# Optimization experiments

Hardware: AMD Instinct MI355X
Metric: run time of the kernel (lower is better)

## Reference

```python
import jax, jax.numpy as jnp
import numpy as np

B, N, F_IN, F_OUT, H = 8, 1024, 128, 64, 4
EPS = 1e-7
NEG_SLOPE = 0.2


def setup_inputs() -> dict:
    key = jax.random.key(0)
    k_a, k_x, k_w, k_aw, k_ab = jax.random.split(key, 5)
    A = jax.random.randint(k_a, (B, N, N), 0, 2).astype(jnp.float32)
    x = jax.random.normal(k_x, (B, N, F_IN), dtype=jnp.float32)
    # per-head params (stacked over head axis): GAT.W (xavier-normal-ish), attention Linear(2F->1)
    W = jax.random.normal(k_w, (H, F_IN, F_OUT), dtype=jnp.float32) * np.sqrt(2.0 / (F_IN + F_OUT))
    lim = 1.0 / np.sqrt(2 * F_OUT)
    a_w = jax.random.uniform(k_aw, (H, 2 * F_OUT), minval=-lim, maxval=lim, dtype=jnp.float32)
    a_b = jax.random.uniform(k_ab, (H,), minval=-lim, maxval=lim, dtype=jnp.float32)
    return {"A": A, "x": x, "W": W, "a_w": a_w, "a_b": a_b}


def reference(A, x, W, a_w, a_b):
    # Wh: (B, H, N, F_OUT)
    Wh = jnp.einsum('bnf,hfo->bhno', x, W)
    # attention linear on concat([Wh_i, Wh_j]) is separable: a1.Wh_i + a2.Wh_j + b
    a1, a2 = a_w[:, :F_OUT], a_w[:, F_OUT:]
    s_i = jnp.einsum('bhno,ho->bhn', Wh, a1)   # depends on row index i (dim 1 of (B,N,N))
    s_j = jnp.einsum('bhno,ho->bhn', Wh, a2)   # depends on col index j (dim 2)
    e = s_i[:, :, :, None] + s_j[:, :, None, :] + a_b[None, :, None, None]  # (B,H,Ni,Nj)
    e = jnp.where(e >= 0, e, NEG_SLOPE * e)  # LeakyReLU(0.2)
    # masked softmax as in source: exp, mask by A, normalize over dim=1 of (B,N,N) -> axis 2 here
    exps = jnp.exp(e) * A[:, None, :, :]
    attn = exps / (jnp.sum(exps, axis=2, keepdims=True) + EPS)
    out = jnp.einsum('bhij,bhjo->bhio', attn, Wh)  # matmul over j
    # concat heads on feature dim: (B, N, H*F_OUT)
    return out.transpose(0, 2, 1, 3).reshape(B, N, H * F_OUT)
```

## Files before the change

kernel.cpp:

```cpp
#include <hip/hip_runtime.h>
#include <hip/hip_bf16.h>
#include <hip/hip_fp16.h>

#define BB 8
#define NN 1024
#define FIN 128
#define FOUT 64
#define HH 4
#define EPSV 1e-7f
#define SLOPE 0.2f
#define LOG2E 1.44269504088896340736f

typedef _Float16 v8h __attribute__((ext_vector_type(8)));
typedef _Float16 v4h __attribute__((ext_vector_type(4)));
typedef _Float16 v2h __attribute__((ext_vector_type(2)));
typedef __fp16 v2hf __attribute__((ext_vector_type(2)));
typedef float v4f __attribute__((ext_vector_type(4)));

union U8 { v2h p[4]; v8h v; };
union U2 { v2hf hf; v2h h; };

__device__ __forceinline__ v2h clamp01(v2h x) {
  v2h zero = {(_Float16)0.0f, (_Float16)0.0f};
  v2h one = {(_Float16)1.0f, (_Float16)1.0f};
  return __builtin_elementwise_min(__builtin_elementwise_max(x, zero), one);
}

__device__ __forceinline__ v2h cvt2(float a, float b) {
  U2 u;
  u.hf = __builtin_amdgcn_cvt_pkrtz(a, b);
  return u.h;
}

__device__ __forceinline__ float dot2(v2h a, v2h b, float c) {
  U2 ua, ub;
  ua.h = a;
  ub.h = b;
  return __builtin_amdgcn_fdot2(ua.hf, ub.hf, c, false);
}

__global__ __launch_bounds__(256) void k0_wt(const float* __restrict__ W,
                                             _Float16* __restrict__ Wtt) {
  for (int it = 0; it < 16; ++it) {
    int idx = blockIdx.x * 4096 + it * 256 + threadIdx.x;
    int e = idx & 7, ln = (idx >> 3) & 15, kgg = (idx >> 7) & 15,
        ct = idx >> 11;
    int c = ct * 16 + ln, k = kgg * 8 + e;
    Wtt[idx] = (_Float16)W[(size_t)(c >> 6) * 8192 + k * 64 + (c & 63)];
  }
}

__global__ __launch_bounds__(256) void k1_whm(
    const float* __restrict__ x, const _Float16* __restrict__ Wtt,
    const float* __restrict__ aw, const float* __restrict__ ab,
    _Float16* __restrict__ WhH, float* __restrict__ si2,
    _Float16* __restrict__ tjh, _Float16* __restrict__ djh,
    _Float16* __restrict__ e2jh, float* __restrict__ e2i_t,
    float* __restrict__ di_t) {
  __shared__ _Float16 xs[16][136];
  int tid = threadIdx.x;
#pragma unroll
  for (int t2 = 0; t2 < 2; ++t2) {
    int idx = t2 * 256 + tid;
    int row = idx >> 5, c4 = (idx & 31) * 4;
    float4 v = *(const float4*)(x + ((size_t)blockIdx.x * 16 + row) * FIN + c4);
    v4h hv;
    hv[0] = (_Float16)v.x; hv[1] = (_Float16)v.y;
    hv[2] = (_Float16)v.z; hv[3] = (_Float16)v.w;
    *(v4h*)(&xs[row][c4]) = hv;
  }
  __syncthreads();
  int w = tid >> 6, l = tid & 63;
  int kg = l >> 4, ln = l & 15;
  v4f acc[4] = {{}, {}, {}, {}};
#pragma unroll
  for (int ks = 0; ks < 4; ++ks) {
    v8h af = *(const v8h*)(&xs[ln][ks * 32 + kg * 8]);
    int kgg = ks * 4 + kg;
#pragma unroll
    for (int t = 0; t < 4; ++t) {
      int ct = w * 4 + t;
      v8h bf = *(const v8h*)(Wtt + (((size_t)ct * 16 + kgg) * 16 + ln) * 8);
      acc[t] = __builtin_amdgcn_mfma_f32_16x16x32_f16(af, bf, acc[t], 0, 0, 0);
    }
  }
  float a1v[4], a2v[4];
#pragma unroll
  for (int t = 0; t < 4; ++t) {
    a1v[t] = aw[w * 128 + t * 16 + ln];
    a2v[t] = aw[w * 128 + 64 + t * 16 + ln];
  }
  float abv = ab[w];
#pragma unroll
  for (int r = 0; r < 4; ++r) {
    float v1 = acc[0][r] * a1v[0] + acc[1][r] * a1v[1] +
               acc[2][r] * a1v[2] + acc[3][r] * a1v[3];
    float v2 = acc[0][r] * a2v[0] + acc[1][r] * a2v[1] +
               acc[2][r] * a2v[2] + acc[3][r] * a2v[3];
#pragma unroll
    for (int off = 1; off < 16; off <<= 1) {
      v1 += __shfl_xor(v1, off);
      v2 += __shfl_xor(v2, off);
    }
    if (ln == 0) {
      int gr = blockIdx.x * 16 + kg * 4 + r;
      int b_ = gr >> 10, n_ = gr & 1023;
      size_t row = ((size_t)b_ * HH + w) * NN + n_;
      float v1L = v1 * LOG2E;
      float tjL = (v2 + abv) * LOG2E;
      si2[row] = v1L;
      float e1i = __builtin_amdgcn_exp2f(v1L);
      float e2i = __builtin_amdgcn_exp2f(0.2f * v1L);
      e2i_t[row] = e2i;
      di_t[row] = e1i - e2i;
      float e1j = __builtin_amdgcn_exp2f(tjL);
      float e2j = __builtin_amdgcn_exp2f(0.2f * tjL);
      tjh[row] = (_Float16)tjL;
      e2jh[row] = (_Float16)e2j;
      djh[row] = (_Float16)(e1j - e2j);
    }
  }
#pragma unroll
  for (int t = 0; t < 4; ++t) {
#pragma unroll
    for (int r = 0; r < 4; ++r) {
      int gr = blockIdx.x * 16 + kg * 4 + r;
      int b_ = gr >> 10, n_ = gr & 1023;
      WhH[(((size_t)b_ * HH + w) * NN + n_) * 64 + (t * 16 + ln)] =
          (_Float16)acc[t][r];
    }
  }
}

__global__ __launch_bounds__(256) void kb_colsum_bits(
    const float* __restrict__ A, const float* __restrict__ si2,
    const float* __restrict__ e2i_t, const float* __restrict__ di_t,
    const _Float16* __restrict__ tjh, const _Float16* __restrict__ djh,
    const _Float16* __restrict__ e2jh, float* __restrict__ part,
    unsigned long long* __restrict__ Abits) {
  __shared__ v2h si_p[4][16], di_p[4][16], e2i_p[4][16];
  int b = blockIdx.z, is = blockIdx.y, jt = blockIdx.x;
  int tid = threadIdx.x;
  int w = tid >> 6, lane = tid & 63;
  int j = jt * 256 + tid;
  int i0 = is * 32;
  if (tid < 64) {
    int h = tid >> 4, pp = tid & 15;
    size_t row = ((size_t)(b * HH + h)) * NN + i0 + 2 * pp;
    si_p[h][pp] = cvt2(si2[row], si2[row + 1]);
    di_p[h][pp] = cvt2(di_t[row], di_t[row + 1]);
    e2i_p[h][pp] = cvt2(e2i_t[row], e2i_t[row + 1]);
  }
  __syncthreads();
  v2h tjb[4], djb[4], ejb[4];
#pragma unroll
  for (int h = 0; h < 4; ++h) {
    size_t jr = ((size_t)(b * HH + h)) * NN + j;
    _Float16 t = tjh[jr], d = djh[jr], e = e2jh[jr];
    tjb[h][0] = t; tjb[h][1] = t;
    djb[h][0] = d; djb[h][1] = d;
    ejb[h][0] = e; ejb[h][1] = e;
  }
  v2h big = {(_Float16)4096.0f, (_Float16)4096.0f};
  float acc[4] = {0.f, 0.f, 0.f, 0.f};
  const float* Ap = A + ((size_t)b * NN + i0) * NN + j;
  unsigned long long myword = 0ull;
#pragma unroll
  for (int c = 0; c < 4; ++c) {
    float av[8];
#pragma unroll
    for (int q = 0; q < 8; ++q) av[q] = Ap[(size_t)(c * 8 + q) * NN];
    v2h apk[4];
#pragma unroll
    for (int q = 0; q < 4; ++q) apk[q] = cvt2(av[2 * q], av[2 * q + 1]);
#pragma unroll
    for (int q = 0; q < 8; ++q) {
      unsigned long long m = __ballot(av[q] != 0.0f);
      if (lane == c * 8 + q) myword = m;
    }
#pragma unroll
    for (int h = 0; h < 4; ++h) {
      U8 si4, di4, ei4;
      si4.v = *(const v8h*)&si_p[h][c * 4];
      di4.v = *(const v8h*)&di_p[h][c * 4];
      ei4.v = *(const v8h*)&e2i_p[h][c * 4];
#pragma unroll
      for (int pp = 0; pp < 4; ++pp) {
        v2h f = si4.p[pp] + tjb[h];
        v2h s = clamp01(f * big);
        v2h ei = s * di4.p[pp] + ei4.p[pp];
        v2h ej = s * djb[h] + ejb[h];
        v2h p = ei * ej;
        acc[h] = dot2(p, apk[pp], acc[h]);
      }
    }
  }
  if (lane < 32)
    Abits[((size_t)b * NN + i0 + lane) * 16 + jt * 4 + w] = myword;
#pragma unroll
  for (int h = 0; h < 4; ++h)
    part[((size_t)(is * 32) + b * HH + h) * NN + j] = acc[h];
}

__global__ __launch_bounds__(256) void k3_scale_tr(
    const _Float16* __restrict__ WhH, const float* __restrict__ part,
    _Float16* __restrict__ VTt) {
  __shared__ float rbuf[64];
  __shared__ _Float16 tile[64 * 66];
  int bid = blockIdx.x;
  int b = bid & 7, rest = bid >> 3;
  int h = rest & 3, jt = rest >> 2;
  int bh = b * HH + h, j0 = jt * 64;
  int tid = threadIdx.x;
  if (tid < 64) {
    float s = 0.f;
#pragma unroll
    for (int is = 0; is < 32; ++is)
      s += part[((size_t)(is * 32) + bh) * NN + j0 + tid];
    rbuf[tid] = 1.0f / (s + EPSV);
  }
  __syncthreads();
#pragma unroll
  for (int it = 0; it < 16; ++it) {
    int lin = it * 256 + tid;
    int jj = lin >> 6, o = lin & 63;
    float v = (float)WhH[((size_t)bh * NN + j0 + jj) * 64 + o] * rbuf[jj];
    tile[o * 66 + jj] = (_Float16)v;
  }
  __syncthreads();
#pragma unroll
  for (int it = 0; it < 16; ++it) {
    int lin = it * 256 + tid;
    int o = lin >> 6, jj64 = lin & 63;
    int j = j0 + jj64;
    int jb = j >> 5, jj = j & 31;
    VTt[(((size_t)bh * 32 + jb) * 64 + o) * 32 + jj] = tile[o * 66 + jj64];
  }
}

__global__ __launch_bounds__(512, 4) void k4_pv(
    const unsigned long long* __restrict__ Abits,
    const float* __restrict__ si2, const _Float16* __restrict__ tjh,
    const _Float16* __restrict__ djh, const _Float16* __restrict__ e2jh,
    const float* __restrict__ e2i_t, const float* __restrict__ di_t,
    const _Float16* __restrict__ VTt, float* __restrict__ out) {
  __shared__ unsigned long long Ab[64][17];
  __shared__ _Float16 tjl[2][1024];
  __shared__ _Float16 djl[2][1024];
  __shared__ _Float16 e2jl[2][1024];
  __shared__ _Float16 lut[256][8];
  __shared__ float sil[2][64], e2il[2][64], dil[2][64];
  __shared__ float red[2][2][64][33];
  int bid = blockIdx.x;
  int b = bid & 7, hp = (bid >> 3) & 1, it = bid >> 4;
  int i0 = it * 64;
  int tid = threadIdx.x;
  {
    size_t base = (size_t)(b * HH + hp * 2) * NN;
    const unsigned int* s1 = (const unsigned int*)(tjh + base);
    const unsigned int* s2 = (const unsigned int*)(djh + base);
    const unsigned int* s3 = (const unsigned int*)(e2jh + base);
    unsigned int* d1 = (unsigned int*)&tjl[0][0];
    unsigned int* d2 = (unsigned int*)&djl[0][0];
    unsigned int* d3 = (unsigned int*)&e2jl[0][0];
    d1[tid] = s1[tid]; d1[tid + 512] = s1[tid + 512];
    d2[tid] = s2[tid]; d2[tid + 512] = s2[tid + 512];
    d3[tid] = s3[tid]; d3[tid + 512] = s3[tid + 512];
  }
  if (tid < 128) {
    int hh = tid >> 6, ii = tid & 63;
    size_t row = (size_t)(b * HH + hp * 2 + hh) * NN + i0 + ii;
    sil[hh][ii] = si2[row];
    e2il[hh][ii] = e2i_t[row];
    dil[hh][ii] = di_t[row];
  }
  if (tid < 256) {
#pragma unroll
    for (int e = 0; e < 8; ++e)
      lut[tid][e] = ((tid >> e) & 1) ? (_Float16)1.0f : (_Float16)0.0f;
  }
  {
#pragma unroll
    for (int t2 = 0; t2 < 2; ++t2) {
      int idx = t2 * 512 + tid;
      int row = idx >> 4, word = idx & 15;
      Ab[row][word] = Abits[((size_t)b * NN + i0 + row) * 16 + word];
    }
  }
  __syncthreads();

  int w = tid >> 6, l = tid & 63;
  int hh = w & 1, jq4 = w >> 1;
  int kg = l >> 4, ln = l & 15;
  v2h si_f[4], e2_f[4], di_f[4];
#pragma unroll
  for (int f = 0; f < 4; ++f) {
    _Float16 s = (_Float16)sil[hh][f * 16 + ln];
    _Float16 e = (_Float16)e2il[hh][f * 16 + ln];
    _Float16 d = (_Float16)dil[hh][f * 16 + ln];
    si_f[f][0] = s; si_f[f][1] = s;
    e2_f[f][0] = e; e2_f[f][1] = e;
    di_f[f][0] = d; di_f[f][1] = d;
  }
  v2h big = {(_Float16)4096.0f, (_Float16)4096.0f};
  int bh = b * HH + hp * 2 + hh;
  v4f acc[4][4] = {};
  const _Float16* VTb = VTt + (size_t)bh * 32 * 64 * 32;
  int jbase = jq4 * 256;

  for (int jq = 0; jq < 8; ++jq) {
    int j = jbase + jq * 32 + kg * 8;
    int widx = j >> 6, sh = j & 63;
    U8 tj8, dj8, ej8;
    tj8.v = *(const v8h*)&tjl[hh][j];
    dj8.v = *(const v8h*)&djl[hh][j];
    ej8.v = *(const v8h*)&e2jl[hh][j];
    const _Float16* vb = VTb + (size_t)(j >> 5) * 2048 + kg * 8;
    v8h b0 = *(const v8h*)(vb + (0 * 16 + ln) * 32);
    v8h b1 = *(const v8h*)(vb + (1 * 16 + ln) * 32);
    v8h b2 = *(const v8h*)(vb + (2 * 16 + ln) * 32);
    v8h b3 = *(const v8h*)(vb + (3 * 16 + ln) * 32);
#pragma unroll
    for (int f = 0; f < 4; ++f) {
      unsigned int bits = (unsigned int)(Ab[f * 16 + ln][widx] >> sh) & 0xffu;
      U8 m, af;
      m.v = *(const v8h*)&lut[bits][0];
#pragma unroll
      for (int q = 0; q < 4; ++q) {
        v2h fv = tj8.p[q] + si_f[f];
        v2h s = clamp01(fv * big);
        v2h ej = s * dj8.p[q] + ej8.p[q];
        v2h ei = s * di_f[f] + e2_f[f];
        af.p[q] = ei * ej * m.p[q];
      }
      acc[f][0] =
          __builtin_amdgcn_mfma_f32_16x16x32_f16(af.v, b0, acc[f][0], 0, 0, 0);
      acc[f][1] =
          __builtin_amdgcn_mfma_f32_16x16x32_f16(af.v, b1, acc[f][1], 0, 0, 0);
      acc[f][2] =
          __builtin_amdgcn_mfma_f32_16x16x32_f16(af.v, b2, acc[f][2], 0, 0, 0);
      acc[f][3] =
          __builtin_amdgcn_mfma_f32_16x16x32_f16(af.v, b3, acc[f][3], 0, 0, 0);
    }
  }

#pragma unroll
  for (int pass = 0; pass < 2; ++pass) {
    int fA = pass * 2, fB = pass * 2 + 1;
    if (pass) __syncthreads();
    if (jq4 == 1 || jq4 == 3) {
      int slot = jq4 >> 1;
#pragma unroll
      for (int t = 0; t < 4; ++t)
#pragma unroll
        for (int r = 0; r < 4; ++r) {
          red[hh][slot][l][t * 4 + r] = acc[fA][t][r];
          red[hh][slot][l][16 + t * 4 + r] = acc[fB][t][r];
        }
    }
    __syncthreads();
    if (jq4 == 0 || jq4 == 2) {
      int slot = jq4 >> 1;
#pragma unroll
      for (int t = 0; t < 4; ++t)
#pragma unroll
        for (int r = 0; r < 4; ++r) {
          acc[fA][t][r] += red[hh][slot][l][t * 4 + r];
          acc[fB][t][r] += red[hh][slot][l][16 + t * 4 + r];
        }
    }
    __syncthreads();
    if (jq4 == 2) {
#pragma unroll
      for (int t = 0; t < 4; ++t)
#pragma unroll
        for (int r = 0; r < 4; ++r) {
          red[hh][0][l][t * 4 + r] = acc[fA][t][r];
          red[hh][0][l][16 + t * 4 + r] = acc[fB][t][r];
        }
    }
    __syncthreads();
    if (jq4 == 0) {
#pragma unroll
      for (int t = 0; t < 4; ++t)
#pragma unroll
        for (int r = 0; r < 4; ++r) {
          acc[fA][t][r] += red[hh][0][l][t * 4 + r];
          acc[fB][t][r] += red[hh][0][l][16 + t * 4 + r];
        }
#pragma unroll
      for (int r = 0; r < 4; ++r) {
        int giA = i0 + fA * 16 + kg * 4 + r;
        float* opA = out + ((size_t)b * NN + giA) * 256 + (hp * 2 + hh) * 64;
        opA[0 * 16 + ln] = acc[fA][0][r];
        opA[1 * 16 + ln] = acc[fA][1][r];
        opA[2 * 16 + ln] = acc[fA][2][r];
        opA[3 * 16 + ln] = acc[fA][3][r];
        float* opB = opA + 16 * 256;
        opB[0 * 16 + ln] = acc[fB][0][r];
        opB[1 * 16 + ln] = acc[fB][1][r];
        opB[2 * 16 + ln] = acc[fB][2][r];
        opB[3 * 16 + ln] = acc[fB][3][r];
      }
    }
  }
}

extern "C" void kernel_launch(void* const* d_in, const int* in_sizes, int n_in,
                              void* d_out, int out_size, void* d_ws,
                              size_t ws_size, hipStream_t stream) {
  const float* A = (const float*)d_in[0];
  const float* x = (const float*)d_in[1];
  const float* W = (const float*)d_in[2];
  const float* aw = (const float*)d_in[3];
  const float* ab = (const float*)d_in[4];
  float* out = (float*)d_out;
  char* ws = (char*)d_ws;
  _Float16* WhH = (_Float16*)ws;
  _Float16* VTt = (_Float16*)(ws + (4u << 20));
  _Float16* Wtt = (_Float16*)(ws + (8u << 20));
  float* si2 = (float*)(ws + (8u << 20) + (256u << 10));
  float* part = (float*)(ws + (8u << 20) + (512u << 10));
  unsigned long long* Abits =
      (unsigned long long*)(ws + (12u << 20) + (512u << 10));
  char* tb = ws + (13u << 20) + (512u << 10);
  _Float16* tjh = (_Float16*)tb;
  _Float16* djh = (_Float16*)(tb + (64u << 10));
  _Float16* e2jh = (_Float16*)(tb + (128u << 10));
  float* e2i_t = (float*)(tb + (192u << 10));
  float* di_t = (float*)(tb + (320u << 10));

  hipLaunchKernelGGL(k0_wt, dim3(8), dim3(256), 0, stream, W, Wtt);
  hipLaunchKernelGGL(k1_whm, dim3(512), dim3(256), 0, stream, x, Wtt, aw, ab,
                     WhH, si2, tjh, djh, e2jh, e2i_t, di_t);
  hipLaunchKernelGGL(kb_colsum_bits, dim3(4, 32, BB), dim3(256), 0, stream, A,
                     si2, e2i_t, di_t, tjh, djh, e2jh, part, Abits);
  hipLaunchKernelGGL(k3_scale_tr, dim3(512), dim3(256), 0, stream, WhH, part,
                     VTt);
  hipLaunchKernelGGL(k4_pv, dim3(256), dim3(512), 0, stream, Abits, si2, tjh,
                     djh, e2jh, e2i_t, di_t, VTt, out);
}
```

Before: 44.73 us.

## Remove scale-transpose kernel by writing transposed Wh and folding normalization into P

The first kernel now writes Wh directly in the transposed tile layout the PV kernel reads, and zeroes a column-sum buffer. The colsum kernel accumulates into that buffer with atomicAdd instead of writing per-slice partials. The PV kernel folds the 1/colsum normalization into the per-column dj/e2j factors rather than scaling V. Together these remove the k3 launch and its partial-sum reduction and transpose traffic. In exchange, the colsum kernel adds float atomics, and rounding changes because the scale is now applied in fp16 before the product.

```diff
diff --git a/kernel.cpp b/kernel.cpp
--- a/kernel.cpp
+++ b/kernel.cpp
@@ -53,17 +53,19 @@
 __global__ __launch_bounds__(256) void k1_whm(
     const float* __restrict__ x, const _Float16* __restrict__ Wtt,
     const float* __restrict__ aw, const float* __restrict__ ab,
-    _Float16* __restrict__ WhH, float* __restrict__ si2,
+    _Float16* __restrict__ WhTt, float* __restrict__ si2,
     _Float16* __restrict__ tjh, _Float16* __restrict__ djh,
     _Float16* __restrict__ e2jh, float* __restrict__ e2i_t,
-    float* __restrict__ di_t) {
+    float* __restrict__ di_t, float* __restrict__ colsum) {
   __shared__ _Float16 xs[16][136];
   int tid = threadIdx.x;
+  int bid = blockIdx.x;
+  if (tid < 64) colsum[bid * 64 + tid] = 0.0f;
 #pragma unroll
   for (int t2 = 0; t2 < 2; ++t2) {
     int idx = t2 * 256 + tid;
     int row = idx >> 5, c4 = (idx & 31) * 4;
-    float4 v = *(const float4*)(x + ((size_t)blockIdx.x * 16 + row) * FIN + c4);
+    float4 v = *(const float4*)(x + ((size_t)bid * 16 + row) * FIN + c4);
     v4h hv;
     hv[0] = (_Float16)v.x; hv[1] = (_Float16)v.y;
     hv[2] = (_Float16)v.z; hv[3] = (_Float16)v.w;
@@ -103,7 +105,7 @@
       v2 += __shfl_xor(v2, off);
     }
     if (ln == 0) {
-      int gr = blockIdx.x * 16 + kg * 4 + r;
+      int gr = bid * 16 + kg * 4 + r;
       int b_ = gr >> 10, n_ = gr & 1023;
       size_t row = ((size_t)b_ * HH + w) * NN + n_;
       float v1L = v1 * LOG2E;
@@ -120,14 +122,18 @@
       djh[row] = (_Float16)(e1j - e2j);
     }
   }
-#pragma unroll
-  for (int t = 0; t < 4; ++t) {
-#pragma unroll
-    for (int r = 0; r < 4; ++r) {
-      int gr = blockIdx.x * 16 + kg * 4 + r;
-      int b_ = gr >> 10, n_ = gr & 1023;
-      WhH[(((size_t)b_ * HH + w) * NN + n_) * 64 + (t * 16 + ln)] =
-          (_Float16)acc[t][r];
+  {
+    int b_ = bid >> 6;
+    int bh = b_ * HH + w;
+    int jb = (bid & 63) >> 1;
+    int jj0 = (bid & 1) * 16 + kg * 4;
+#pragma unroll
+    for (int t = 0; t < 4; ++t) {
+      v4h hv;
+#pragma unroll
+      for (int r = 0; r < 4; ++r) hv[r] = (_Float16)acc[t][r];
+      *(v4h*)(WhTt + (((size_t)bh * 32 + jb) * 64 + (t * 16 + ln)) * 32 +
+              jj0) = hv;
     }
   }
 }
@@ -136,7 +142,7 @@
     const float* __restrict__ A, const float* __restrict__ si2,
     const float* __restrict__ e2i_t, const float* __restrict__ di_t,
     const _Float16* __restrict__ tjh, const _Float16* __restrict__ djh,
-    const _Float16* __restrict__ e2jh, float* __restrict__ part,
+    const _Float16* __restrict__ e2jh, float* __restrict__ colsum,
     unsigned long long* __restrict__ Abits) {
   __shared__ v2h si_p[4][16], di_p[4][16], e2i_p[4][16];
   int b = blockIdx.z, is = blockIdx.y, jt = blockIdx.x;
@@ -199,43 +205,7 @@
     Abits[((size_t)b * NN + i0 + lane) * 16 + jt * 4 + w] = myword;
 #pragma unroll
   for (int h = 0; h < 4; ++h)
-    part[((size_t)(is * 32) + b * HH + h) * NN + j] = acc[h];
-}
-
-__global__ __launch_bounds__(256) void k3_scale_tr(
-    const _Float16* __restrict__ WhH, const float* __restrict__ part,
-    _Float16* __restrict__ VTt) {
-  __shared__ float rbuf[64];
-  __shared__ _Float16 tile[64 * 66];
-  int bid = blockIdx.x;
-  int b = bid & 7, rest = bid >> 3;
-  int h = rest & 3, jt = rest >> 2;
-  int bh = b * HH + h, j0 = jt * 64;
-  int tid = threadIdx.x;
-  if (tid < 64) {
-    float s = 0.f;
-#pragma unroll
-    for (int is = 0; is < 32; ++is)
-      s += part[((size_t)(is * 32) + bh) * NN + j0 + tid];
-    rbuf[tid] = 1.0f / (s + EPSV);
-  }
-  __syncthreads();
-#pragma unroll
-  for (int it = 0; it < 16; ++it) {
-    int lin = it * 256 + tid;
-    int jj = lin >> 6, o = lin & 63;
-    float v = (float)WhH[((size_t)bh * NN + j0 + jj) * 64 + o] * rbuf[jj];
-    tile[o * 66 + jj] = (_Float16)v;
-  }
-  __syncthreads();
-#pragma unroll
-  for (int it = 0; it < 16; ++it) {
-    int lin = it * 256 + tid;
-    int o = lin >> 6, jj64 = lin & 63;
-    int j = j0 + jj64;
-    int jb = j >> 5, jj = j & 31;
-    VTt[(((size_t)bh * 32 + jb) * 64 + o) * 32 + jj] = tile[o * 66 + jj64];
-  }
+    atomicAdd(&colsum[((size_t)(b * HH + h)) * NN + j], acc[h]);
 }
 
 __global__ __launch_bounds__(512, 4) void k4_pv(
@@ -243,7 +213,8 @@
     const float* __restrict__ si2, const _Float16* __restrict__ tjh,
     const _Float16* __restrict__ djh, const _Float16* __restrict__ e2jh,
     const float* __restrict__ e2i_t, const float* __restrict__ di_t,
-    const _Float16* __restrict__ VTt, float* __restrict__ out) {
+    const _Float16* __restrict__ WhTt, const float* __restrict__ colsum,
+    float* __restrict__ out) {
   __shared__ unsigned long long Ab[64][17];
   __shared__ _Float16 tjl[2][1024];
   __shared__ _Float16 djl[2][1024];
@@ -257,15 +228,16 @@
   int tid = threadIdx.x;
   {
     size_t base = (size_t)(b * HH + hp * 2) * NN;
-    const unsigned int* s1 = (const unsigned int*)(tjh + base);
-    const unsigned int* s2 = (const unsigned int*)(djh + base);
-    const unsigned int* s3 = (const unsigned int*)(e2jh + base);
-    unsigned int* d1 = (unsigned int*)&tjl[0][0];
-    unsigned int* d2 = (unsigned int*)&djl[0][0];
-    unsigned int* d3 = (unsigned int*)&e2jl[0][0];
-    d1[tid] = s1[tid]; d1[tid + 512] = s1[tid + 512];
-    d2[tid] = s2[tid]; d2[tid + 512] = s2[tid + 512];
-    d3[tid] = s3[tid]; d3[tid + 512] = s3[tid + 512];
+#pragma unroll
+    for (int t2 = 0; t2 < 4; ++t2) {
+      int idx = t2 * 512 + tid;
+      int hh = idx >> 10, j = idx & 1023;
+      size_t row = base + (size_t)hh * NN + j;
+      float rr = 1.0f / (colsum[row] + EPSV);
+      tjl[hh][j] = tjh[row];
+      djl[hh][j] = (_Float16)((float)djh[row] * rr);
+      e2jl[hh][j] = (_Float16)((float)e2jh[row] * rr);
+    }
   }
   if (tid < 128) {
     int hh = tid >> 6, ii = tid & 63;
@@ -305,7 +277,7 @@
   v2h big = {(_Float16)4096.0f, (_Float16)4096.0f};
   int bh = b * HH + hp * 2 + hh;
   v4f acc[4][4] = {};
-  const _Float16* VTb = VTt + (size_t)bh * 32 * 64 * 32;
+  const _Float16* VTb = WhTt + (size_t)bh * 32 * 64 * 32;
   int jbase = jq4 * 256;
 
   for (int jq = 0; jq < 8; ++jq) {
@@ -416,14 +388,13 @@
   const float* ab = (const float*)d_in[4];
   float* out = (float*)d_out;
   char* ws = (char*)d_ws;
-  _Float16* WhH = (_Float16*)ws;
-  _Float16* VTt = (_Float16*)(ws + (4u << 20));
-  _Float16* Wtt = (_Float16*)(ws + (8u << 20));
-  float* si2 = (float*)(ws + (8u << 20) + (256u << 10));
-  float* part = (float*)(ws + (8u << 20) + (512u << 10));
+  _Float16* WhTt = (_Float16*)ws;
+  _Float16* Wtt = (_Float16*)(ws + (4u << 20));
+  float* si2 = (float*)(ws + (4u << 20) + (64u << 10));
+  float* colsum = (float*)(ws + (4u << 20) + (192u << 10));
   unsigned long long* Abits =
-      (unsigned long long*)(ws + (12u << 20) + (512u << 10));
-  char* tb = ws + (13u << 20) + (512u << 10);
+      (unsigned long long*)(ws + (4u << 20) + (320u << 10));
+  char* tb = ws + (5u << 20) + (320u << 10);
   _Float16* tjh = (_Float16*)tb;
   _Float16* djh = (_Float16*)(tb + (64u << 10));
   _Float16* e2jh = (_Float16*)(tb + (128u << 10));
@@ -432,11 +403,9 @@
 
   hipLaunchKernelGGL(k0_wt, dim3(8), dim3(256), 0, stream, W, Wtt);
   hipLaunchKernelGGL(k1_whm, dim3(512), dim3(256), 0, stream, x, Wtt, aw, ab,
-                     WhH, si2, tjh, djh, e2jh, e2i_t, di_t);
+                     WhTt, si2, tjh, djh, e2jh, e2i_t, di_t, colsum);
   hipLaunchKernelGGL(kb_colsum_bits, dim3(4, 32, BB), dim3(256), 0, stream, A,
-                     si2, e2i_t, di_t, tjh, djh, e2jh, part, Abits);
-  hipLaunchKernelGGL(k3_scale_tr, dim3(512), dim3(256), 0, stream, WhH, part,
-                     VTt);
+                     si2, e2i_t, di_t, tjh, djh, e2jh, colsum, Abits);
   hipLaunchKernelGGL(k4_pv, dim3(256), dim3(512), 0, stream, Abits, si2, tjh,
-                     djh, e2jh, e2i_t, di_t, VTt, out);
-}
+                     djh, e2jh, e2i_t, di_t, WhTt, colsum, out);
+}
```

Result: faster. 41.20 us, median of 2 (-7.9%).
